# Optimization experiments

Hardware: AMD Instinct MI355X
Metric: run time of the kernel (lower is better)

Reference implementation:

```python
import jax, jax.numpy as jnp
import numpy as np

N_NODES = 50000
N_EDGES = 600000
H_DIM = 128
BN_EPS = 1e-5


def setup_inputs() -> dict:
    key = jax.random.key(0)
    k1, k2, k3, k4 = jax.random.split(key, 4)
    ent_emb = jax.random.normal(k1, (N_NODES, H_DIM), dtype=jnp.float32)
    # xavier_normal_ init for the 128x128 weight
    std = float(np.sqrt(2.0 / (H_DIM + H_DIM)))
    neigh_w = jax.random.normal(k2, (H_DIM, H_DIM), dtype=jnp.float32) * std
    gamma = jnp.ones((H_DIM,), dtype=jnp.float32)
    beta = jnp.zeros((H_DIM,), dtype=jnp.float32)
    src = jax.random.randint(k3, (N_EDGES,), 0, N_NODES, dtype=jnp.int32)
    dst = jax.random.randint(k4, (N_EDGES,), 0, N_NODES, dtype=jnp.int32)
    return {"ent_emb": ent_emb, "neigh_w": neigh_w, "gamma": gamma,
            "beta": beta, "src": src, "dst": dst}


def reference(ent_emb, neigh_w, gamma, beta, src, dst):
    # Edge dot-product scores: u_dot_v('emb','emb')  -> [E]
    e_src = ent_emb[src]                      # [E, H]
    e_dst = ent_emb[dst]                      # [E, H]
    scores = jnp.sum(e_src * e_dst, axis=-1)  # [E]

    # edge_softmax: softmax over incoming edges of each destination node
    seg_max = jax.ops.segment_max(scores, dst, num_segments=N_NODES)
    seg_max = jnp.where(jnp.isfinite(seg_max), seg_max, 0.0)  # nodes w/o edges
    e = jnp.exp(scores - seg_max[dst])                         # [E]
    seg_sum = jax.ops.segment_sum(e, dst, num_segments=N_NODES)
    norm = e / seg_sum[dst]                                    # [E]

    # update_all(u_mul_e, sum): weighted gather-sum aggregation
    msg = e_src * norm[:, None]                                # [E, H]
    neigh = jax.ops.segment_sum(msg, dst, num_segments=N_NODES)  # [N, H]

    # matmul + BatchNorm1d (training-mode batch stats) + tanh
    h = neigh @ neigh_w                                        # [N, H]
    mean = jnp.mean(h, axis=0)
    var = jnp.var(h, axis=0)  # biased, matches torch BN normalization
    h = (h - mean) * jax.lax.rsqrt(var + BN_EPS) * gamma + beta
    return jnp.tanh(h)
```

## Files before the change

### kernel.cpp

```cpp
#include <hip/hip_runtime.h>
#include <hip/hip_fp16.h>
#include <math.h>

#define N_NODES 50000
#define N_EDGES 600000
#define H 128
#define BN_EPS 1e-5f
#define MAXDEG 48

__global__ void k_scatter(const int* __restrict__ src, const int* __restrict__ dst,
                          int* __restrict__ cnt, int* __restrict__ slots,
                          const float* __restrict__ emb, __half* __restrict__ emb16) {
    int i = blockIdx.x * blockDim.x + threadIdx.x;
    if (i < N_EDGES) {
        int d = dst[i];
        int pos = atomicAdd(cnt + d, 1);
        if (pos < MAXDEG) slots[d * MAXDEG + pos] = src[i];
    }
    if (i < N_NODES * H / 8) {
        float4 f0 = ((const float4*)emb)[2 * i];
        float4 f1 = ((const float4*)emb)[2 * i + 1];
        union { uint4 u; __half2 h2[4]; } U;
        U.h2[0] = __floats2half2_rn(f0.x, f0.y);
        U.h2[1] = __floats2half2_rn(f0.z, f0.w);
        U.h2[2] = __floats2half2_rn(f1.x, f1.y);
        U.h2[3] = __floats2half2_rn(f1.z, f1.w);
        ((uint4*)emb16)[i] = U.u;
    }
}

#define F4SCALE(a, s) { (a).x *= (s); (a).y *= (s); (a).z *= (s); (a).w *= (s); }
#define F4FMA(a, e, v) { (a).x += (e)*(v).x; (a).y += (e)*(v).y; (a).z += (e)*(v).z; (a).w += (e)*(v).w; }
#define F4SHFLADD(a, msk) { (a).x += __shfl_xor((a).x, msk, 64); (a).y += __shfl_xor((a).y, msk, 64); \
                            (a).z += __shfl_xor((a).z, msk, 64); (a).w += __shfl_xor((a).w, msk, 64); }

__global__ __launch_bounds__(256) void k_fused(const float* __restrict__ emb,
                                               const __half* __restrict__ emb16,
                                               const int* __restrict__ cnt,
                                               const int* __restrict__ slots,
                                               __half* __restrict__ neigh) {
    int wid = (blockIdx.x * blockDim.x + threadIdx.x) >> 6;
    int lane = threadIdx.x & 63;
    if (wid >= N_NODES) return;
    int g = lane >> 3;
    int l = lane & 7;

    int deg = min(cnt[wid], MAXDEG);
    int sid = slots[wid * MAXDEG + min(lane, MAXDEG - 1)];

    const float4* rd = (const float4*)(emb + (size_t)wid * H) + l * 4;
    float4 b0 = rd[0], b1 = rd[1], b2 = rd[2], b3 = rd[3];

    float m = -INFINITY, ssum = 0.0f;
    float4 acc0 = {0,0,0,0}, acc1 = {0,0,0,0}, acc2 = {0,0,0,0}, acc3 = {0,0,0,0};

    for (int cb = 0; cb < deg; cb += 8) {
        int e = cb + g;
        bool valid = e < deg;
        int s = __shfl(sid, valid ? e : 0, 64);
        const uint4* rs = (const uint4*)(emb16 + (size_t)s * H) + l * 2;
        uint4 p0 = rs[0], p1 = rs[1];
        const __half2* h0 = (const __half2*)&p0;
        const __half2* h1 = (const __half2*)&p1;
        float2 t0 = __half22float2(h0[0]), t1 = __half22float2(h0[1]);
        float2 t2 = __half22float2(h0[2]), t3 = __half22float2(h0[3]);
        float2 t4 = __half22float2(h1[0]), t5 = __half22float2(h1[1]);
        float2 t6 = __half22float2(h1[2]), t7 = __half22float2(h1[3]);
        float4 a0 = make_float4(t0.x, t0.y, t1.x, t1.y);
        float4 a1 = make_float4(t2.x, t2.y, t3.x, t3.y);
        float4 a2 = make_float4(t4.x, t4.y, t5.x, t5.y);
        float4 a3 = make_float4(t6.x, t6.y, t7.x, t7.y);

        float v = a0.x*b0.x + a0.y*b0.y + a0.z*b0.z + a0.w*b0.w
                + a1.x*b1.x + a1.y*b1.y + a1.z*b1.z + a1.w*b1.w
                + a2.x*b2.x + a2.y*b2.y + a2.z*b2.z + a2.w*b2.w
                + a3.x*b3.x + a3.y*b3.y + a3.z*b3.z + a3.w*b3.w;
        v += __shfl_xor(v, 1, 64);
        v += __shfl_xor(v, 2, 64);
        v += __shfl_xor(v, 4, 64);
        if (!valid) v = -INFINITY;

        float cmax = v;
        cmax = fmaxf(cmax, __shfl_xor(cmax, 8, 64));
        cmax = fmaxf(cmax, __shfl_xor(cmax, 16, 64));
        cmax = fmaxf(cmax, __shfl_xor(cmax, 32, 64));
        float mnew = fmaxf(m, cmax);
        if (mnew > m) {
            float scale = __expf(m - mnew);
            ssum *= scale;
            F4SCALE(acc0, scale); F4SCALE(acc1, scale);
            F4SCALE(acc2, scale); F4SCALE(acc3, scale);
            m = mnew;
        }

        float ev = __expf(v - m);
        ssum += ev;
        F4FMA(acc0, ev, a0); F4FMA(acc1, ev, a1);
        F4FMA(acc2, ev, a2); F4FMA(acc3, ev, a3);
    }

    ssum += __shfl_xor(ssum, 8, 64);
    ssum += __shfl_xor(ssum, 16, 64);
    ssum += __shfl_xor(ssum, 32, 64);
    F4SHFLADD(acc0, 8);  F4SHFLADD(acc1, 8);  F4SHFLADD(acc2, 8);  F4SHFLADD(acc3, 8);
    F4SHFLADD(acc0, 16); F4SHFLADD(acc1, 16); F4SHFLADD(acc2, 16); F4SHFLADD(acc3, 16);
    F4SHFLADD(acc0, 32); F4SHFLADD(acc1, 32); F4SHFLADD(acc2, 32); F4SHFLADD(acc3, 32);

    float inv = (deg > 0) ? 1.0f / ssum : 0.0f;
    if (g == 0) {
        F4SCALE(acc0, inv); F4SCALE(acc1, inv); F4SCALE(acc2, inv); F4SCALE(acc3, inv);
        union { uint4 u; __half2 h2[4]; } U0, U1;
        U0.h2[0] = __floats2half2_rn(acc0.x, acc0.y);
        U0.h2[1] = __floats2half2_rn(acc0.z, acc0.w);
        U0.h2[2] = __floats2half2_rn(acc1.x, acc1.y);
        U0.h2[3] = __floats2half2_rn(acc1.z, acc1.w);
        U1.h2[0] = __floats2half2_rn(acc2.x, acc2.y);
        U1.h2[1] = __floats2half2_rn(acc2.z, acc2.w);
        U1.h2[2] = __floats2half2_rn(acc3.x, acc3.y);
        U1.h2[3] = __floats2half2_rn(acc3.z, acc3.w);
        uint4* po = (uint4*)(neigh + (size_t)wid * H);
        po[2 * l] = U0.u;
        po[2 * l + 1] = U1.u;
    }
}

#define MM_ROWS 128
__global__ __launch_bounds__(256, 2) void k_matmul(const __half* __restrict__ neigh,
                                                   const float* __restrict__ W,
                                                   __half* __restrict__ hout,
                                                   float* __restrict__ stats) {
    __shared__ float Wl[H * H];
    int t = threadIdx.x;
    int n0 = blockIdx.x * MM_ROWS;
    int cg = t & 15, rg = t >> 4;
    int j0 = cg * 8;
    int r0 = n0 + rg * 8;

    for (int idx = t; idx < H * H / 4; idx += 256)
        ((float4*)Wl)[idx] = ((const float4*)W)[idx];

    const __half* pr[8];
    bool valid[8];
#pragma unroll
    for (int i = 0; i < 8; ++i) {
        int n = r0 + i;
        valid[i] = (n < N_NODES);
        pr[i] = neigh + (size_t)(valid[i] ? n : 0) * H;
    }

    __syncthreads();

    float acc[8][8] = {};
    for (int k0 = 0; k0 < H; k0 += 4) {
        uint2 rv[8];
#pragma unroll
        for (int i = 0; i < 8; ++i) rv[i] = *(const uint2*)(pr[i] + k0);
        float rf[8][4];
#pragma unroll
        for (int i = 0; i < 8; ++i) {
            const __half2* hp = (const __half2*)&rv[i];
            float2 x0 = __half22float2(hp[0]);
            float2 x1 = __half22float2(hp[1]);
            rf[i][0] = x0.x; rf[i][1] = x0.y; rf[i][2] = x1.x; rf[i][3] = x1.y;
        }
        float4 wa[4], wb[4];
#pragma unroll
        for (int kk = 0; kk < 4; ++kk) {
            wa[kk] = *(const float4*)&Wl[(k0 + kk) * H + j0];
            wb[kk] = *(const float4*)&Wl[(k0 + kk) * H + j0 + 4];
        }
#pragma unroll
        for (int kk = 0; kk < 4; ++kk) {
#pragma unroll
            for (int i = 0; i < 8; ++i) {
                float rk = rf[i][kk];
                acc[i][0] += rk * wa[kk].x;
                acc[i][1] += rk * wa[kk].y;
                acc[i][2] += rk * wa[kk].z;
                acc[i][3] += rk * wa[kk].w;
                acc[i][4] += rk * wb[kk].x;
                acc[i][5] += rk * wb[kk].y;
                acc[i][6] += rk * wb[kk].z;
                acc[i][7] += rk * wb[kk].w;
            }
        }
    }

#pragma unroll
    for (int i = 0; i < 8; ++i) {
        if (valid[i]) {
            union { uint4 u; __half2 h2[4]; } U;
            U.h2[0] = __floats2half2_rn(acc[i][0], acc[i][1]);
            U.h2[1] = __floats2half2_rn(acc[i][2], acc[i][3]);
            U.h2[2] = __floats2half2_rn(acc[i][4], acc[i][5]);
            U.h2[3] = __floats2half2_rn(acc[i][6], acc[i][7]);
            *(uint4*)(hout + (size_t)(r0 + i) * H + j0) = U.u;
        }
    }

    __syncthreads();
    float* Sl = Wl;
    float* Ql = Wl + 16 * H;
#pragma unroll
    for (int c = 0; c < 8; ++c) {
        float s = 0.0f, q = 0.0f;
#pragma unroll
        for (int i = 0; i < 8; ++i) {
            if (valid[i]) { s += acc[i][c]; q += acc[i][c] * acc[i][c]; }
        }
        Sl[rg * H + j0 + c] = s;
        Ql[rg * H + j0 + c] = q;
    }
    __syncthreads();
    if (t < H) {
        float s = 0.0f;
#pragma unroll
        for (int r = 0; r < 16; ++r) s += Sl[r * H + t];
        atomicAdd(stats + t, s);
    } else {
        int j = t - H;
        float q = 0.0f;
#pragma unroll
        for (int r = 0; r < 16; ++r) q += Ql[r * H + j];
        atomicAdd(stats + 128 + j, q);
    }
}

__device__ __forceinline__ float tanh_fast(float x) {
    float e = __expf(2.0f * x);
    return 1.0f - 2.0f / (e + 1.0f);
}

__global__ __launch_bounds__(256) void k_apply_f16(const __half* __restrict__ h,
                                                   float* __restrict__ out,
                                                   const float* __restrict__ stats,
                                                   const float* __restrict__ gamma,
                                                   const float* __restrict__ beta) {
    __shared__ float sc[128], sh[128];
    int t = threadIdx.x;
    if (t < 128) {
        float mean = stats[t] * (1.0f / N_NODES);
        float var = stats[128 + t] * (1.0f / N_NODES) - mean * mean;
        var = fmaxf(var, 0.0f);
        float s = gamma[t] * rsqrtf(var + BN_EPS);
        sc[t] = s;
        sh[t] = beta[t] - mean * s;
    }
    __syncthreads();
    int i = blockIdx.x * 256 + t;
    if (i < N_NODES * H / 8) {
        union { uint4 u; __half2 h2[4]; } U;
        U.u = ((const uint4*)h)[i];
        int jb = (i & 15) * 8;
        float2 f0 = __half22float2(U.h2[0]);
        float2 f1 = __half22float2(U.h2[1]);
        float2 f2 = __half22float2(U.h2[2]);
        float2 f3 = __half22float2(U.h2[3]);
        float4 o0, o1;
        o0.x = tanh_fast(f0.x * sc[jb]     + sh[jb]);
        o0.y = tanh_fast(f0.y * sc[jb + 1] + sh[jb + 1]);
        o0.z = tanh_fast(f1.x * sc[jb + 2] + sh[jb + 2]);
        o0.w = tanh_fast(f1.y * sc[jb + 3] + sh[jb + 3]);
        o1.x = tanh_fast(f2.x * sc[jb + 4] + sh[jb + 4]);
        o1.y = tanh_fast(f2.y * sc[jb + 5] + sh[jb + 5]);
        o1.z = tanh_fast(f3.x * sc[jb + 6] + sh[jb + 6]);
        o1.w = tanh_fast(f3.y * sc[jb + 7] + sh[jb + 7]);
        ((float4*)out)[2 * i]     = o0;
        ((float4*)out)[2 * i + 1] = o1;
    }
}

extern "C" void kernel_launch(void* const* d_in, const int* in_sizes, int n_in,
                              void* d_out, int out_size, void* d_ws, size_t ws_size,
                              hipStream_t stream) {
    const float* emb   = (const float*)d_in[0];
    const float* W     = (const float*)d_in[1];
    const float* gamma = (const float*)d_in[2];
    const float* beta  = (const float*)d_in[3];
    const int*   src   = (const int*)d_in[4];
    const int*   dst   = (const int*)d_in[5];
    float* out = (float*)d_out;

    int*    cnt    = (int*)d_ws;
    float*  stats  = (float*)(cnt + N_NODES);
    int*    slots  = (int*)(stats + 256) + 4;
    __half* neigh  = (__half*)(slots + (size_t)N_NODES * MAXDEG);
    __half* hbuf   = neigh + (size_t)N_NODES * H;
    __half* emb16  = hbuf + (size_t)N_NODES * H;

    hipMemsetAsync(cnt, 0, (N_NODES + 260) * sizeof(int), stream);
    int nthr_sc = (N_NODES * H / 8 > N_EDGES) ? N_NODES * H / 8 : N_EDGES;
    k_scatter<<<(nthr_sc + 255) / 256, 256, 0, stream>>>(src, dst, cnt, slots, emb, emb16);
    k_fused<<<(N_NODES * 64 + 255) / 256, 256, 0, stream>>>(emb, emb16, cnt, slots, neigh);
    int nblk_mm = (N_NODES + MM_ROWS - 1) / MM_ROWS;
    k_matmul<<<nblk_mm, 256, 0, stream>>>(neigh, W, hbuf, stats);
    k_apply_f16<<<(N_NODES * H / 8 + 255) / 256, 256, 0, stream>>>(hbuf, out, stats, gamma, beta);
}
```

Before: 211.3 us.

## Use fp16 packed dot2 matmul with pre-converted weights and ushort neighbor slots

Pre-converts W to packed fp16 pairs inside the scatter kernel and rewrites the matmul inner loop to use the fdot2 instruction on half2 operands. It also halves the LDS footprint and the rows per block so more blocks fit per CU. Neighbor slot indices are stored as 16-bit values to cut scatter and gather traffic. The fp16 weights lower matmul precision. Node ids up to 49999 fit in an unsigned short.

```diff
diff --git a/kernel.cpp b/kernel.cpp
--- a/kernel.cpp
+++ b/kernel.cpp
@@ -8,14 +8,31 @@
 #define BN_EPS 1e-5f
 #define MAXDEG 48
 
+typedef unsigned short ushort_t;
+typedef unsigned int uint_t;
+
+static __device__ __forceinline__ float dot2f(uint_t au, uint_t bu, float c) {
+#if __has_builtin(__builtin_amdgcn_fdot2)
+    typedef _Float16 f16x2 __attribute__((ext_vector_type(2)));
+    return __builtin_amdgcn_fdot2(__builtin_bit_cast(f16x2, au),
+                                  __builtin_bit_cast(f16x2, bu), c, false);
+#else
+    __half2 a = __builtin_bit_cast(__half2, au);
+    __half2 b = __builtin_bit_cast(__half2, bu);
+    float2 af = __half22float2(a), bf = __half22float2(b);
+    return c + af.x * bf.x + af.y * bf.y;
+#endif
+}
+
 __global__ void k_scatter(const int* __restrict__ src, const int* __restrict__ dst,
-                          int* __restrict__ cnt, int* __restrict__ slots,
-                          const float* __restrict__ emb, __half* __restrict__ emb16) {
+                          int* __restrict__ cnt, ushort_t* __restrict__ slots,
+                          const float* __restrict__ emb, __half* __restrict__ emb16,
+                          const float* __restrict__ W, uint_t* __restrict__ w16p) {
     int i = blockIdx.x * blockDim.x + threadIdx.x;
     if (i < N_EDGES) {
         int d = dst[i];
         int pos = atomicAdd(cnt + d, 1);
-        if (pos < MAXDEG) slots[d * MAXDEG + pos] = src[i];
+        if (pos < MAXDEG) slots[d * MAXDEG + pos] = (ushort_t)src[i];
     }
     if (i < N_NODES * H / 8) {
         float4 f0 = ((const float4*)emb)[2 * i];
@@ -27,6 +44,19 @@
         U.h2[3] = __floats2half2_rn(f1.z, f1.w);
         ((uint4*)emb16)[i] = U.u;
     }
+    if (i < H * H / 8) {
+        int e  = 4 * i;
+        int k2 = e >> 7;
+        int j  = e & 127;
+        float4 w0 = *(const float4*)(W + (size_t)(2 * k2) * H + j);
+        float4 w1 = *(const float4*)(W + (size_t)(2 * k2 + 1) * H + j);
+        union { uint4 u; __half2 h2[4]; } U;
+        U.h2[0] = __floats2half2_rn(w0.x, w1.x);
+        U.h2[1] = __floats2half2_rn(w0.y, w1.y);
+        U.h2[2] = __floats2half2_rn(w0.z, w1.z);
+        U.h2[3] = __floats2half2_rn(w0.w, w1.w);
+        ((uint4*)w16p)[i] = U.u;
+    }
 }
 
 #define F4SCALE(a, s) { (a).x *= (s); (a).y *= (s); (a).z *= (s); (a).w *= (s); }
@@ -37,7 +67,7 @@
 __global__ __launch_bounds__(256) void k_fused(const float* __restrict__ emb,
                                                const __half* __restrict__ emb16,
                                                const int* __restrict__ cnt,
-                                               const int* __restrict__ slots,
+                                               const ushort_t* __restrict__ slots,
                                                __half* __restrict__ neigh) {
     int wid = (blockIdx.x * blockDim.x + threadIdx.x) >> 6;
     int lane = threadIdx.x & 63;
@@ -124,25 +154,25 @@
     }
 }
 
-#define MM_ROWS 128
-__global__ __launch_bounds__(256, 2) void k_matmul(const __half* __restrict__ neigh,
-                                                   const float* __restrict__ W,
+#define MM_ROWS 64
+__global__ __launch_bounds__(256, 4) void k_matmul(const __half* __restrict__ neigh,
+                                                   const uint_t* __restrict__ w16p,
                                                    __half* __restrict__ hout,
                                                    float* __restrict__ stats) {
-    __shared__ float Wl[H * H];
+    __shared__ uint_t Wl[(H / 2) * H];
     int t = threadIdx.x;
     int n0 = blockIdx.x * MM_ROWS;
     int cg = t & 15, rg = t >> 4;
     int j0 = cg * 8;
-    int r0 = n0 + rg * 8;
-
-    for (int idx = t; idx < H * H / 4; idx += 256)
-        ((float4*)Wl)[idx] = ((const float4*)W)[idx];
-
-    const __half* pr[8];
-    bool valid[8];
-#pragma unroll
-    for (int i = 0; i < 8; ++i) {
+    int r0 = n0 + rg * 4;
+
+    for (int idx = t; idx < H * H / 8; idx += 256)
+        ((uint4*)Wl)[idx] = ((const uint4*)w16p)[idx];
+
+    const __half* pr[4];
+    bool valid[4];
+#pragma unroll
+    for (int i = 0; i < 4; ++i) {
         int n = r0 + i;
         valid[i] = (n < N_NODES);
         pr[i] = neigh + (size_t)(valid[i] ? n : 0) * H;
@@ -150,44 +180,33 @@
 
     __syncthreads();
 
-    float acc[8][8] = {};
-    for (int k0 = 0; k0 < H; k0 += 4) {
-        uint2 rv[8];
-#pragma unroll
-        for (int i = 0; i < 8; ++i) rv[i] = *(const uint2*)(pr[i] + k0);
-        float rf[8][4];
-#pragma unroll
-        for (int i = 0; i < 8; ++i) {
-            const __half2* hp = (const __half2*)&rv[i];
-            float2 x0 = __half22float2(hp[0]);
-            float2 x1 = __half22float2(hp[1]);
-            rf[i][0] = x0.x; rf[i][1] = x0.y; rf[i][2] = x1.x; rf[i][3] = x1.y;
-        }
-        float4 wa[4], wb[4];
+    float acc[4][8] = {};
+    for (int k2 = 0; k2 < H / 2; k2 += 4) {
+        uint4 rv[4];
+#pragma unroll
+        for (int i = 0; i < 4; ++i) rv[i] = *(const uint4*)(pr[i] + 2 * k2);
 #pragma unroll
         for (int kk = 0; kk < 4; ++kk) {
-            wa[kk] = *(const float4*)&Wl[(k0 + kk) * H + j0];
-            wb[kk] = *(const float4*)&Wl[(k0 + kk) * H + j0 + 4];
-        }
-#pragma unroll
-        for (int kk = 0; kk < 4; ++kk) {
-#pragma unroll
-            for (int i = 0; i < 8; ++i) {
-                float rk = rf[i][kk];
-                acc[i][0] += rk * wa[kk].x;
-                acc[i][1] += rk * wa[kk].y;
-                acc[i][2] += rk * wa[kk].z;
-                acc[i][3] += rk * wa[kk].w;
-                acc[i][4] += rk * wb[kk].x;
-                acc[i][5] += rk * wb[kk].y;
-                acc[i][6] += rk * wb[kk].z;
-                acc[i][7] += rk * wb[kk].w;
+            const uint4* wp = (const uint4*)&Wl[(k2 + kk) * H + j0];
+            uint4 wA = wp[0];
+            uint4 wB = wp[1];
+#pragma unroll
+            for (int i = 0; i < 4; ++i) {
+                uint_t a = ((const uint_t*)&rv[i])[kk];
+                acc[i][0] = dot2f(a, wA.x, acc[i][0]);
+                acc[i][1] = dot2f(a, wA.y, acc[i][1]);
+                acc[i][2] = dot2f(a, wA.z, acc[i][2]);
+                acc[i][3] = dot2f(a, wA.w, acc[i][3]);
+                acc[i][4] = dot2f(a, wB.x, acc[i][4]);
+                acc[i][5] = dot2f(a, wB.y, acc[i][5]);
+                acc[i][6] = dot2f(a, wB.z, acc[i][6]);
+                acc[i][7] = dot2f(a, wB.w, acc[i][7]);
             }
         }
     }
 
 #pragma unroll
-    for (int i = 0; i < 8; ++i) {
+    for (int i = 0; i < 4; ++i) {
         if (valid[i]) {
             union { uint4 u; __half2 h2[4]; } U;
             U.h2[0] = __floats2half2_rn(acc[i][0], acc[i][1]);
@@ -199,13 +218,13 @@
     }
 
     __syncthreads();
-    float* Sl = Wl;
-    float* Ql = Wl + 16 * H;
+    float* Sl = (float*)Wl;
+    float* Ql = (float*)Wl + 16 * H;
 #pragma unroll
     for (int c = 0; c < 8; ++c) {
         float s = 0.0f, q = 0.0f;
 #pragma unroll
-        for (int i = 0; i < 8; ++i) {
+        for (int i = 0; i < 4; ++i) {
             if (valid[i]) { s += acc[i][c]; q += acc[i][c] * acc[i][c]; }
         }
         Sl[rg * H + j0 + c] = s;
@@ -281,18 +300,19 @@
     const int*   dst   = (const int*)d_in[5];
     float* out = (float*)d_out;
 
-    int*    cnt    = (int*)d_ws;
-    float*  stats  = (float*)(cnt + N_NODES);
-    int*    slots  = (int*)(stats + 256) + 4;
-    __half* neigh  = (__half*)(slots + (size_t)N_NODES * MAXDEG);
-    __half* hbuf   = neigh + (size_t)N_NODES * H;
-    __half* emb16  = hbuf + (size_t)N_NODES * H;
+    int*      cnt   = (int*)d_ws;
+    float*    stats = (float*)(cnt + N_NODES);
+    ushort_t* slots = (ushort_t*)((int*)(stats + 256) + 4);
+    __half*   neigh = (__half*)(slots + (size_t)N_NODES * MAXDEG);
+    __half*   hbuf  = neigh + (size_t)N_NODES * H;
+    __half*   emb16 = hbuf + (size_t)N_NODES * H;
+    uint_t*   w16p  = (uint_t*)(emb16 + (size_t)N_NODES * H);
 
     hipMemsetAsync(cnt, 0, (N_NODES + 260) * sizeof(int), stream);
     int nthr_sc = (N_NODES * H / 8 > N_EDGES) ? N_NODES * H / 8 : N_EDGES;
-    k_scatter<<<(nthr_sc + 255) / 256, 256, 0, stream>>>(src, dst, cnt, slots, emb, emb16);
+    k_scatter<<<(nthr_sc + 255) / 256, 256, 0, stream>>>(src, dst, cnt, slots, emb, emb16, W, w16p);
     k_fused<<<(N_NODES * 64 + 255) / 256, 256, 0, stream>>>(emb, emb16, cnt, slots, neigh);
     int nblk_mm = (N_NODES + MM_ROWS - 1) / MM_ROWS;
-    k_matmul<<<nblk_mm, 256, 0, stream>>>(neigh, W, hbuf, stats);
+    k_matmul<<<nblk_mm, 256, 0, stream>>>(neigh, w16p, hbuf, stats);
     k_apply_f16<<<(N_NODES * H / 8 + 255) / 256, 256, 0, stream>>>(hbuf, out, stats, gamma, beta);
 }
```

After: 203.1 us. -3.9%, faster.
